# Kernel optimization log

Measured on AMD Instinct MI355X. Metric: run time of the kernel, lower is better.

Reference implementation:

```python
import jax, jax.numpy as jnp
import numpy as np

# Static tree structure: B jets, each a perfect binary tree of depth DEPTH.
B = 64
DEPTH = 12                       # levels 0..DEPTH; level j has B*2**j nodes
N_FEAT = 7
N_HID = 128
LEVEL_SIZES = [B * (1 << j) for j in range(DEPTH + 1)]
OFFSETS = np.concatenate([[0], np.cumsum(LEVEL_SIZES)]).astype(np.int64).tolist()
TOTAL = OFFSETS[-1]              # 524224 nodes
INNER_SIZES = LEVEL_SIZES[:-1]   # all nodes inner except leaf level
INNER_OFF = np.concatenate([[0], np.cumsum(INNER_SIZES)]).astype(np.int64).tolist()


def setup_inputs() -> dict:
    key = jax.random.key(0)
    k_c, k_wu, k_wh = jax.random.split(key, 3)
    contents = jax.random.normal(k_c, (TOTAL, N_FEAT), dtype=jnp.float32)
    # children: per level j < DEPTH, a random pairing (permutation) of level j+1 nodes
    rng = np.random.default_rng(0)
    ch = []
    for j in range(DEPTH):
        perm = rng.permutation(LEVEL_SIZES[j + 1]).astype(np.int32)
        ch.append(perm.reshape(LEVEL_SIZES[j], 2))
    children = jnp.asarray(np.concatenate(ch, axis=0))  # [262080, 2]
    # Learned params (torch nn.Linear: y = x @ W.T + b)
    w_u = jax.random.normal(k_wu, (N_HID, N_FEAT), dtype=jnp.float32) / np.float32(np.sqrt(N_FEAT))
    b_u = jnp.zeros((N_HID,), jnp.float32)
    w_h = jax.random.normal(k_wh, (N_HID, 3 * N_HID), dtype=jnp.float32) / np.float32(np.sqrt(3 * N_HID))
    b_h = jnp.zeros((N_HID,), jnp.float32)
    return {"contents": contents, "children": children,
            "w_u": w_u, "b_u": b_u, "w_h": w_h, "b_h": b_h}


def reference(contents, children, w_u, b_u, w_h, b_h):
    # Bottom-up pass over tree levels (leaves -> root), mirroring the torch loop
    # over levels[::-1]. Perfect binary tree: every non-leaf node is inner.
    emb = None
    for j in range(DEPTH, -1, -1):
        c_j = contents[OFFSETS[j]:OFFSETS[j + 1]]              # [B*2^j, F]
        u = jnp.tanh(c_j @ w_u.T + b_u)                        # [B*2^j, H]
        if j < DEPTH:
            ch_j = children[INNER_OFF[j]:INNER_OFF[j + 1]]     # [B*2^j, 2]
            h_L = emb[ch_j[:, 0]]                              # gather from prev level
            h_R = emb[ch_j[:, 1]]
            emb = jnp.tanh(jnp.concatenate([h_L, h_R, u], axis=1) @ w_h.T + b_h)
        else:
            emb = u  # leaf level: no inner nodes
    return emb.reshape(B, -1)  # root embedding per jet: [B, N_HID]
```

## Files before the change

### kernel.cpp

```cpp
#include <hip/hip_runtime.h>
#include <hip/hip_bf16.h>


#define NF 7
#define NH 128
#define XSTR 136
#define XSTR3 392

typedef __bf16 bf16;
typedef __bf16 bf16x8 __attribute__((ext_vector_type(8)));
typedef float floatx16 __attribute__((ext_vector_type(16)));

__device__ __forceinline__ float ftanh(float x){
    float e = __expf(2.0f * x);
    return 1.0f - __fdividef(2.0f, e + 1.0f);
}

__global__ __launch_bounds__(256) void k_prep(
    const float* __restrict__ contents, const int2* __restrict__ children,
    const float* __restrict__ w_u, const float* __restrict__ b_u,
    const float* __restrict__ w_h,
    unsigned int* __restrict__ usm_u32, int* __restrict__ ids_A,
    int* __restrict__ ids_B, bf16* __restrict__ wb, bf16* __restrict__ w_ub)
{
    __shared__ float csL[128 * 8];
    const int t = threadIdx.x;
    const int b = blockIdx.x;

    if (b >= 512){
        if (b == 512){
            if (t < 64){
                int root = t;
                int* base = ids_B + root * 32;
                const int2* ch0 = children;
                const int2* ch1 = children + 64;
                const int2* ch2 = children + 192;
                const int2* ch3 = children + 448;
                int l1[2], l2[4], l3[8];
                { int2 c = ch0[root]; l1[0] = c.x; l1[1] = c.y; }
                #pragma unroll
                for (int k = 0; k < 2; ++k){ int2 c = ch1[l1[k]]; l2[2*k] = c.x; l2[2*k+1] = c.y; }
                #pragma unroll
                for (int k = 0; k < 4; ++k){ int2 c = ch2[l2[k]]; l3[2*k] = c.x; l3[2*k+1] = c.y; }
                base[0] = root;
                base[1] = l1[0]; base[2] = l1[1];
                #pragma unroll
                for (int k = 0; k < 4; ++k) base[3 + k] = l2[k];
                #pragma unroll
                for (int k = 0; k < 8; ++k) base[7 + k] = l3[k];
                #pragma unroll
                for (int k = 0; k < 8; ++k){
                    int2 c = ch3[l3[k]];
                    base[15 + 2*k] = c.x; base[16 + 2*k] = c.y;
                }
            } else if (t < 192){
                int col = t - 64;
                union { uint4 u4[2]; bf16 h[16]; } row;
                #pragma unroll
                for (int f = 0; f < NF; ++f) row.h[f] = (bf16)w_u[col * NF + f];
                row.h[7] = (bf16)b_u[col];
                #pragma unroll
                for (int k = 8; k < 16; ++k) row.h[k] = (bf16)0.0f;
                *(uint4*)&w_ub[col * 16]     = row.u4[0];
                *(uint4*)&w_ub[col * 16 + 8] = row.u4[1];
            }
        } else if (b < 517){
            int root = (b - 513) * 256 + t;
            int* base = ids_A + root * 128;
            const int2* ch4 = children + 960;
            const int2* ch5 = children + 1984;
            const int2* ch6 = children + 4032;
            const int2* ch7 = children + 8128;
            const int2* ch8 = children + 16320;
            const int2* ch9 = children + 32704;
            int l5[2], l6[4], l7[8], l8[16], l9[32];
            { int2 c = ch4[root]; l5[0] = c.x; l5[1] = c.y; }
            #pragma unroll
            for (int k = 0; k < 2; ++k){ int2 c = ch5[l5[k]]; l6[2*k] = c.x; l6[2*k+1] = c.y; }
            #pragma unroll
            for (int k = 0; k < 4; ++k){ int2 c = ch6[l6[k]]; l7[2*k] = c.x; l7[2*k+1] = c.y; }
            #pragma unroll
            for (int k = 0; k < 8; ++k){ int2 c = ch7[l7[k]]; l8[2*k] = c.x; l8[2*k+1] = c.y; }
            #pragma unroll
            for (int k = 0; k < 16; ++k){ int2 c = ch8[l8[k]]; l9[2*k] = c.x; l9[2*k+1] = c.y; }
            base[0] = root;
            base[1] = l5[0]; base[2] = l5[1];
            #pragma unroll
            for (int k = 0; k < 4; ++k)  base[3 + k]  = l6[k];
            #pragma unroll
            for (int k = 0; k < 8; ++k)  base[7 + k]  = l7[k];
            #pragma unroll
            for (int k = 0; k < 16; ++k) base[15 + k] = l8[k];
            #pragma unroll
            for (int k = 0; k < 32; ++k) base[31 + k] = l9[k];
            #pragma unroll
            for (int k = 0; k < 32; ++k){
                int2 c = ch9[l9[k]];
                base[63 + 2*k] = c.x; base[64 + 2*k] = c.y;
            }
        } else {
            int idx = (b - 517) * 256 + t;
            wb[idx] = (bf16)w_h[idx];
        }
        return;
    }

    const size_t srow = (size_t)b * 128;
    if (t < 224){
        float4 v = ((const float4*)(contents + srow * NF))[t];
        int e = t * 4;
        float vv[4] = {v.x, v.y, v.z, v.w};
        #pragma unroll
        for (int r = 0; r < 4; ++r){ int ee = e + r; csL[(ee/7)*8 + (ee%7)] = vv[r]; }
    }
    const int cp = t & 63;
    const int quarter = t >> 6;
    float wu0[NF], wu1[NF];
    const float* w0 = w_u + (size_t)(2 * cp) * NF;
    #pragma unroll
    for (int f = 0; f < NF; ++f){ wu0[f] = w0[f]; wu1[f] = w0[NF + f]; }
    const float bu0 = b_u[2 * cp], bu1 = b_u[2 * cp + 1];
    __syncthreads();
    #pragma unroll 4
    for (int i = 0; i < 32; ++i){
        int node = quarter * 32 + i;
        float4 c0 = *(const float4*)&csL[node * 8];
        float4 c1 = *(const float4*)&csL[node * 8 + 4];
        float a0 = bu0, a1 = bu1;
        a0 = fmaf(c0.x, wu0[0], a0); a1 = fmaf(c0.x, wu1[0], a1);
        a0 = fmaf(c0.y, wu0[1], a0); a1 = fmaf(c0.y, wu1[1], a1);
        a0 = fmaf(c0.z, wu0[2], a0); a1 = fmaf(c0.z, wu1[2], a1);
        a0 = fmaf(c0.w, wu0[3], a0); a1 = fmaf(c0.w, wu1[3], a1);
        a0 = fmaf(c1.x, wu0[4], a0); a1 = fmaf(c1.x, wu1[4], a1);
        a0 = fmaf(c1.y, wu0[5], a0); a1 = fmaf(c1.y, wu1[5], a1);
        a0 = fmaf(c1.z, wu0[6], a0); a1 = fmaf(c1.z, wu1[6], a1);
        union { unsigned int u; bf16 h[2]; } pk;
        pk.h[0] = (bf16)ftanh(a0);
        pk.h[1] = (bf16)ftanh(a1);
        usm_u32[(srow + node) * 64 + cp] = pk.u;
    }
}

__global__ __launch_bounds__(256, 2) void k_lvl11(
    const float* __restrict__ contents, const int2* __restrict__ children,
    const bf16* __restrict__ w_ub, const bf16* __restrict__ wb,
    const float* __restrict__ b_h, bf16* __restrict__ emb11)
{
    __shared__ bf16 xs[64 * XSTR3];
    __shared__ bf16 ca[192 * 16];
    __shared__ int chS[128];
    const int t = threadIdx.x;
    const int node0 = blockIdx.x * 64;
    const int2* ch11 = children + 131008;
    const float* cont11 = contents + (size_t)131008 * NF;
    const float* contL  = contents + (size_t)262080 * NF;

    if (t < 64){ int2 c = ch11[node0 + t]; chS[2*t] = c.x; chS[2*t + 1] = c.y; }
    __syncthreads();

    if (t < 192){
        const float* src = (t < 128) ? (contL + (size_t)chS[t] * NF)
                                     : (cont11 + (size_t)(node0 + t - 128) * NF);
        union { uint4 u4[2]; bf16 h[16]; } row;
        #pragma unroll
        for (int f = 0; f < NF; ++f) row.h[f] = (bf16)src[f];
        row.h[7] = (bf16)1.0f;
        #pragma unroll
        for (int k = 8; k < 16; ++k) row.h[k] = (bf16)0.0f;
        *(uint4*)&ca[t * 16]     = row.u4[0];
        *(uint4*)&ca[t * 16 + 8] = row.u4[1];
    }

    const int lane = t & 63;
    const int ct = t >> 6;
    const int m = lane & 31;
    const int q = lane >> 5;
    const int colg = ct * 32 + m;
    const bf16x8 bu = *(const bf16x8*)(w_ub + (size_t)colg * 16 + q * 8);
    __syncthreads();

    #pragma unroll
    for (int tile = 0; tile < 6; ++tile){
        bf16x8 a = *(const bf16x8*)&ca[(tile * 32 + m) * 16 + q * 8];
        floatx16 acc = {0,0,0,0,0,0,0,0,0,0,0,0,0,0,0,0};
        acc = __builtin_amdgcn_mfma_f32_32x32x16_bf16(a, bu, acc, 0, 0, 0);
        #pragma unroll
        for (int r = 0; r < 16; ++r){
            int row = (r & 3) + 8 * (r >> 2) + 4 * q;
            bf16 hv = (bf16)ftanh(acc[r]);
            if (tile < 4){
                int c = tile * 32 + row;
                xs[(c >> 1) * XSTR3 + (c & 1) * 128 + colg] = hv;
            } else {
                int i = (tile - 4) * 32 + row;
                xs[i * XSTR3 + 256 + colg] = hv;
            }
        }
    }
    __syncthreads();

    floatx16 acc0 = {0,0,0,0,0,0,0,0,0,0,0,0,0,0,0,0};
    floatx16 acc1 = {0,0,0,0,0,0,0,0,0,0,0,0,0,0,0,0};
    const bf16* bq = wb + (size_t)colg * 384 + q * 8;
    const bf16* xa = &xs[m * XSTR3 + q * 8];
    #pragma unroll
    for (int grp = 0; grp < 3; ++grp){
        bf16x8 bfr[8];
        #pragma unroll
        for (int kk = 0; kk < 8; ++kk)
            bfr[kk] = *(const bf16x8*)(bq + grp * 128 + kk * 16);
        #pragma unroll
        for (int kk = 0; kk < 8; ++kk){
            bf16x8 a0 = *(const bf16x8*)(xa + grp * 128 + kk * 16);
            bf16x8 a1 = *(const bf16x8*)(xa + grp * 128 + kk * 16 + 32 * XSTR3);
            acc0 = __builtin_amdgcn_mfma_f32_32x32x16_bf16(a0, bfr[kk], acc0, 0, 0, 0);
            acc1 = __builtin_amdgcn_mfma_f32_32x32x16_bf16(a1, bfr[kk], acc1, 0, 0, 0);
        }
    }

    const float bv = b_h[colg];
    #pragma unroll
    for (int nt = 0; nt < 2; ++nt){
        const floatx16* accp = nt ? &acc1 : &acc0;
        #pragma unroll
        for (int r = 0; r < 16; ++r){
            int row  = (r & 3) + 8 * (r >> 2) + 4 * q;
            int node = node0 + nt * 32 + row;
            emb11[(size_t)node * NH + colg] = (bf16)ftanh((*accp)[r] + bv);
        }
    }
}

__global__ __launch_bounds__(256, 4) void k_inner(
    const int2* __restrict__ children, const float* __restrict__ contents,
    const float* __restrict__ w_u, const float* __restrict__ b_u,
    const bf16* __restrict__ wb, const float* __restrict__ b_h,
    const bf16* __restrict__ emb_next, bf16* __restrict__ out_b)
{
    __shared__ bf16 xs[64 * XSTR];
    __shared__ int2 ch_s[64];
    __shared__ float cs[64 * 8];
    const int t = threadIdx.x;
    const int block0 = blockIdx.x * 64;
    if (t < 64) ch_s[t] = children[block0 + t];
    if (t < 112){
        float4 v = ((const float4*)(contents + (size_t)block0 * NF))[t];
        int e = t * 4;
        float vv[4] = {v.x, v.y, v.z, v.w};
        #pragma unroll
        for (int r = 0; r < 4; ++r){ int ee = e + r; cs[(ee/7)*8 + (ee%7)] = vv[r]; }
    }
    const int cp = t & 63;
    const int quarter = t >> 6;
    float wu0[NF], wu1[NF];
    {
        const float* w0 = w_u + (size_t)(2 * cp) * NF;
        #pragma unroll
        for (int f = 0; f < NF; ++f){ wu0[f] = w0[f]; wu1[f] = w0[NF + f]; }
    }
    const float bu0 = b_u[2 * cp], bu1 = b_u[2 * cp + 1];
    const int lane = t & 63;
    const int ct = t >> 6;
    const int m = lane & 31;
    const int q = lane >> 5;
    floatx16 acc0 = {0,0,0,0,0,0,0,0,0,0,0,0,0,0,0,0};
    floatx16 acc1 = {0,0,0,0,0,0,0,0,0,0,0,0,0,0,0,0};
    const bf16* bq = wb + ((size_t)(ct * 32 + m) * 384 + q * 8);
    #pragma unroll 1
    for (int p = 0; p < 3; ++p){
        __syncthreads();
        if (p < 2){
            #pragma unroll
            for (int r = 0; r < 4; ++r){
                int task = r * 256 + t;
                int i = task >> 4, part = task & 15;
                int row = (p == 0) ? ch_s[i].x : ch_s[i].y;
                uint4 v = *(const uint4*)(emb_next + (size_t)row * NH + part * 8);
                *(uint4*)&xs[i * XSTR + part * 8] = v;
            }
        } else {
            #pragma unroll 4
            for (int i = 0; i < 16; ++i){
                int node = quarter * 16 + i;
                float4 c0 = *(const float4*)&cs[node * 8];
                float4 c1 = *(const float4*)&cs[node * 8 + 4];
                float a0 = bu0, a1 = bu1;
                a0 = fmaf(c0.x, wu0[0], a0); a1 = fmaf(c0.x, wu1[0], a1);
                a0 = fmaf(c0.y, wu0[1], a0); a1 = fmaf(c0.y, wu1[1], a1);
                a0 = fmaf(c0.z, wu0[2], a0); a1 = fmaf(c0.z, wu1[2], a1);
                a0 = fmaf(c0.w, wu0[3], a0); a1 = fmaf(c0.w, wu1[3], a1);
                a0 = fmaf(c1.x, wu0[4], a0); a1 = fmaf(c1.x, wu1[4], a1);
                a0 = fmaf(c1.y, wu0[5], a0); a1 = fmaf(c1.y, wu1[5], a1);
                a0 = fmaf(c1.z, wu0[6], a0); a1 = fmaf(c1.z, wu1[6], a1);
                union { unsigned int u; bf16 h[2]; } pk;
                pk.h[0] = (bf16)ftanh(a0);
                pk.h[1] = (bf16)ftanh(a1);
                ((unsigned int*)xs)[node * (XSTR / 2) + cp] = pk.u;
            }
        }
        bf16x8 bfr[8];
        #pragma unroll
        for (int kk = 0; kk < 8; ++kk)
            bfr[kk] = *(const bf16x8*)(bq + p * 128 + kk * 16);
        __syncthreads();
        const bf16* xa = &xs[m * XSTR + q * 8];
        #pragma unroll
        for (int kk = 0; kk < 8; ++kk){
            bf16x8 a0 = *(const bf16x8*)(xa + kk * 16);
            bf16x8 a1 = *(const bf16x8*)(xa + kk * 16 + 32 * XSTR);
            acc0 = __builtin_amdgcn_mfma_f32_32x32x16_bf16(a0, bfr[kk], acc0, 0, 0, 0);
            acc1 = __builtin_amdgcn_mfma_f32_32x32x16_bf16(a1, bfr[kk], acc1, 0, 0, 0);
        }
    }
    const int colg = ct * 32 + m;
    const float bv = b_h[colg];
    #pragma unroll
    for (int nt = 0; nt < 2; ++nt){
        const floatx16* accp = nt ? &acc1 : &acc0;
        #pragma unroll
        for (int r = 0; r < 16; ++r){
            int row  = (r & 3) + 8 * (r >> 2) + 4 * q;
            int node = block0 + nt * 32 + row;
            out_b[(size_t)node * NH + colg] = (bf16)ftanh((*accp)[r] + bv);
        }
    }
}

__global__ __launch_bounds__(256, 2) void k_tailA(
    const int* __restrict__ ids_A, const bf16* __restrict__ u_small,
    const bf16* __restrict__ wb, const float* __restrict__ b_h,
    const bf16* __restrict__ emb10, bf16* __restrict__ emb4)
{
    __shared__ bf16 xs[32 * XSTR3];
    __shared__ bf16 embL[32 * 136];
    __shared__ int ids[128];
    const int t = threadIdx.x, root = blockIdx.x;
    const int ct = t >> 6, lane = t & 63, m = lane & 31, q = lane >> 5;
    const float bv = b_h[ct * 32 + m];
    if (t < 32) ((uint4*)ids)[t] = ((const uint4*)(ids_A + root * 128))[t];
    __syncthreads();
    const bf16* bq = wb + ((size_t)(ct * 32 + m) * 384 + q * 8);

    #pragma unroll 1
    for (int l = 9; l >= 4; --l){
        const int n = 1 << (l - 4);
        #pragma unroll 1
        for (int r = 0; r < 4; ++r){
            int task = r * 256 + t;
            if (task < n * 32){
                int i = task >> 5, half = (task >> 4) & 1, part = task & 15;
                uint4 v;
                if (l == 9) v = *(const uint4*)(emb10 + (size_t)ids[63 + 2*i + half] * NH + part * 8);
                else        v = *(uint4*)&embL[(2*i + half) * 136 + part * 8];
                *(uint4*)&xs[i * XSTR3 + half * 128 + part * 8] = v;
            }
        }
        #pragma unroll 1
        for (int r = 0; r < 2; ++r){
            int task = r * 256 + t;
            if (task < n * 16){
                int i = task >> 4, part = task & 15;
                size_t row = (size_t)64 * ((1u << l) - 1) + ids[(n - 1) + i];
                *(uint4*)&xs[i * XSTR3 + 256 + part * 8] =
                    *(const uint4*)(u_small + row * NH + part * 8);
            }
        }
        __syncthreads();
        floatx16 accs[3];
        #pragma unroll
        for (int g = 0; g < 3; ++g) accs[g] = (floatx16){0,0,0,0,0,0,0,0,0,0,0,0,0,0,0,0};
        const bf16* xa = &xs[m * XSTR3 + q * 8];
        #pragma unroll
        for (int grp = 0; grp < 3; ++grp){
            bf16x8 bfr[8];
            #pragma unroll
            for (int kk = 0; kk < 8; ++kk)
                bfr[kk] = *(const bf16x8*)(bq + grp * 128 + kk * 16);
            #pragma unroll
            for (int kk = 0; kk < 8; ++kk){
                bf16x8 a0 = *(const bf16x8*)(xa + grp * 128 + kk * 16);
                accs[grp] = __builtin_amdgcn_mfma_f32_32x32x16_bf16(a0, bfr[kk], accs[grp], 0, 0, 0);
            }
        }
        floatx16 acc = accs[0] + accs[1] + accs[2];
        __syncthreads();
        #pragma unroll
        for (int r = 0; r < 16; ++r){
            int row = (r & 3) + 8 * (r >> 2) + 4 * q;
            if (row < n){
                float v = ftanh(acc[r] + bv);
                if (l > 4) embL[row * 136 + ct * 32 + m] = (bf16)v;
                else       emb4[(size_t)root * NH + ct * 32 + m] = (bf16)v;
            }
        }
        __syncthreads();
    }
}

__global__ __launch_bounds__(256, 2) void k_tailB(
    const int* __restrict__ ids_B, const bf16* __restrict__ u_small,
    const bf16* __restrict__ wb, const float* __restrict__ b_h,
    const bf16* __restrict__ emb4, float* __restrict__ out_f)
{
    __shared__ bf16 xs[8 * XSTR3];
    __shared__ bf16 embL[8 * 136];
    __shared__ int ids[32];
    const int t = threadIdx.x, root = blockIdx.x;
    const int ct = t >> 6, lane = t & 63, m = lane & 31, q = lane >> 5;
    const float bv = b_h[ct * 32 + m];
    if (t < 8) ((uint4*)ids)[t] = ((const uint4*)(ids_B + root * 32))[t];
    __syncthreads();
    const bf16* bq = wb + ((size_t)(ct * 32 + m) * 384 + q * 8);

    #pragma unroll 1
    for (int l = 3; l >= 0; --l){
        const int n = 1 << l;
        {
            int task = t;
            if (task < n * 32){
                int i = task >> 5, half = (task >> 4) & 1, part = task & 15;
                uint4 v;
                if (l == 3) v = *(const uint4*)(emb4 + (size_t)ids[15 + 2*i + half] * NH + part * 8);
                else        v = *(uint4*)&embL[(2*i + half) * 136 + part * 8];
                *(uint4*)&xs[i * XSTR3 + half * 128 + part * 8] = v;
            }
            if (task < n * 16){
                int i = task >> 4, part = task & 15;
                size_t row = (size_t)64 * ((1u << l) - 1) + ids[(n - 1) + i];
                *(uint4*)&xs[i * XSTR3 + 256 + part * 8] =
                    *(const uint4*)(u_small + row * NH + part * 8);
            }
        }
        __syncthreads();
        floatx16 accs[3];
        #pragma unroll
        for (int g = 0; g < 3; ++g) accs[g] = (floatx16){0,0,0,0,0,0,0,0,0,0,0,0,0,0,0,0};
        const bf16* xa = &xs[m * XSTR3 + q * 8];
        #pragma unroll
        for (int grp = 0; grp < 3; ++grp){
            bf16x8 bfr[8];
            #pragma unroll
            for (int kk = 0; kk < 8; ++kk)
                bfr[kk] = *(const bf16x8*)(bq + grp * 128 + kk * 16);
            #pragma unroll
            for (int kk = 0; kk < 8; ++kk){
                bf16x8 a0 = *(const bf16x8*)(xa + grp * 128 + kk * 16);
                accs[grp] = __builtin_amdgcn_mfma_f32_32x32x16_bf16(a0, bfr[kk], accs[grp], 0, 0, 0);
            }
        }
        floatx16 acc = accs[0] + accs[1] + accs[2];
        __syncthreads();
        #pragma unroll
        for (int r = 0; r < 16; ++r){
            int row = (r & 3) + 8 * (r >> 2) + 4 * q;
            if (row < n){
                float v = ftanh(acc[r] + bv);
                if (l > 0) embL[row * 136 + ct * 32 + m] = (bf16)v;
                else       out_f[(size_t)root * NH + ct * 32 + m] = v;
            }
        }
        __syncthreads();
    }
}

extern "C" void kernel_launch(void* const* d_in, const int* in_sizes, int n_in,
                              void* d_out, int out_size, void* d_ws, size_t ws_size,
                              hipStream_t stream){
    const float* contents = (const float*)d_in[0];
    const int2*  children = (const int2*)d_in[1];
    const float* w_u      = (const float*)d_in[2];
    const float* b_u      = (const float*)d_in[3];
    const float* w_h      = (const float*)d_in[4];
    const float* b_h      = (const float*)d_in[5];
    float* outf = (float*)d_out;

    bf16* embA    = (bf16*)d_ws;
    bf16* embB    = embA + (size_t)65536 * NH;
    bf16* wb      = embB + (size_t)131072 * NH;
    bf16* u_small = wb + (size_t)NH * 384;
    int*  ids_A   = (int*)(u_small + (size_t)65536 * NH);
    int*  ids_B   = ids_A + 1024 * 128;
    bf16* w_ub    = (bf16*)(ids_B + 64 * 32);

    hipLaunchKernelGGL(k_prep, dim3(709), dim3(256), 0, stream,
                       contents, children, w_u, b_u, w_h,
                       (unsigned int*)u_small, ids_A, ids_B, wb, w_ub);
    hipLaunchKernelGGL(k_lvl11, dim3(2048), dim3(256), 0, stream,
                       contents, children, w_ub, wb, b_h, embB);
    hipLaunchKernelGGL(k_inner, dim3(1024), dim3(256), 0, stream,
                       children + 65472, contents + (size_t)65472 * NF,
                       w_u, b_u, wb, b_h, embB, embA);
    hipLaunchKernelGGL(k_tailA, dim3(1024), dim3(256), 0, stream,
                       ids_A, u_small, wb, b_h, embA, embB);
    hipLaunchKernelGGL(k_tailB, dim3(64), dim3(256), 0, stream,
                       ids_B, u_small, wb, b_h, embB, outf);
}
```

Measured before the change: 223.0 us.

## Fuse prep kernel into level-11 kernel and halve its node tile

Folds the separate preparation kernel (leaf u precompute, index tables, weight bf16 conversion) into the level-11 kernel as extra blocks, removing one launch and its dependency barrier. The level-11 blocks now convert w_u/b_u and w_h to bf16 on the fly from fp32 instead of reading prepared copies. Each block handles 32 nodes instead of 64, doubling the block count, so every block reloads and converts the full W_h slice and per-block weight reuse halves. Extra global traffic and conversion work per block are traded for fewer launches and more parallelism.

```diff
diff --git a/kernel.cpp b/kernel.cpp
--- a/kernel.cpp
+++ b/kernel.cpp
@@ -16,19 +16,92 @@
     return 1.0f - __fdividef(2.0f, e + 1.0f);
 }
 
-__global__ __launch_bounds__(256) void k_prep(
+__global__ __launch_bounds__(256, 2) void k_lvl11(
     const float* __restrict__ contents, const int2* __restrict__ children,
     const float* __restrict__ w_u, const float* __restrict__ b_u,
-    const float* __restrict__ w_h,
+    const float* __restrict__ w_h, const float* __restrict__ b_h,
+    bf16* __restrict__ emb11,
     unsigned int* __restrict__ usm_u32, int* __restrict__ ids_A,
-    int* __restrict__ ids_B, bf16* __restrict__ wb, bf16* __restrict__ w_ub)
+    int* __restrict__ ids_B, bf16* __restrict__ wb)
 {
-    __shared__ float csL[128 * 8];
+    __shared__ bf16 xs[32 * XSTR3];
+    __shared__ bf16 ca[96 * 16];
+    __shared__ int chS[64];
     const int t = threadIdx.x;
     const int b = blockIdx.x;
 
-    if (b >= 512){
-        if (b == 512){
+    if (b >= 4096){
+        if (b < 4608){
+            float* csL = (float*)xs;
+            const size_t srow = (size_t)(b - 4096) * 128;
+            if (t < 224){
+                float4 v = ((const float4*)(contents + srow * NF))[t];
+                int e = t * 4;
+                float vv[4] = {v.x, v.y, v.z, v.w};
+                #pragma unroll
+                for (int r = 0; r < 4; ++r){ int ee = e + r; csL[(ee/7)*8 + (ee%7)] = vv[r]; }
+            }
+            const int cp = t & 63;
+            const int quarter = t >> 6;
+            float wu0[NF], wu1[NF];
+            const float* w0 = w_u + (size_t)(2 * cp) * NF;
+            #pragma unroll
+            for (int f = 0; f < NF; ++f){ wu0[f] = w0[f]; wu1[f] = w0[NF + f]; }
+            const float bu0 = b_u[2 * cp], bu1 = b_u[2 * cp + 1];
+            __syncthreads();
+            #pragma unroll 4
+            for (int i = 0; i < 32; ++i){
+                int node = quarter * 32 + i;
+                float4 c0 = *(const float4*)&csL[node * 8];
+                float4 c1 = *(const float4*)&csL[node * 8 + 4];
+                float a0 = bu0, a1 = bu1;
+                a0 = fmaf(c0.x, wu0[0], a0); a1 = fmaf(c0.x, wu1[0], a1);
+                a0 = fmaf(c0.y, wu0[1], a0); a1 = fmaf(c0.y, wu1[1], a1);
+                a0 = fmaf(c0.z, wu0[2], a0); a1 = fmaf(c0.z, wu1[2], a1);
+                a0 = fmaf(c0.w, wu0[3], a0); a1 = fmaf(c0.w, wu1[3], a1);
+                a0 = fmaf(c1.x, wu0[4], a0); a1 = fmaf(c1.x, wu1[4], a1);
+                a0 = fmaf(c1.y, wu0[5], a0); a1 = fmaf(c1.y, wu1[5], a1);
+                a0 = fmaf(c1.z, wu0[6], a0); a1 = fmaf(c1.z, wu1[6], a1);
+                union { unsigned int u; bf16 h[2]; } pk;
+                pk.h[0] = (bf16)ftanh(a0);
+                pk.h[1] = (bf16)ftanh(a1);
+                usm_u32[(srow + node) * 64 + cp] = pk.u;
+            }
+        } else if (b < 4612){
+            int root = (b - 4608) * 256 + t;
+            int* base = ids_A + root * 128;
+            const int2* ch4 = children + 960;
+            const int2* ch5 = children + 1984;
+            const int2* ch6 = children + 4032;
+            const int2* ch7 = children + 8128;
+            const int2* ch8 = children + 16320;
+            const int2* ch9 = children + 32704;
+            int l5[2], l6[4], l7[8], l8[16], l9[32];
+            { int2 c = ch4[root]; l5[0] = c.x; l5[1] = c.y; }
+            #pragma unroll
+            for (int k = 0; k < 2; ++k){ int2 c = ch5[l5[k]]; l6[2*k] = c.x; l6[2*k+1] = c.y; }
+            #pragma unroll
+            for (int k = 0; k < 4; ++k){ int2 c = ch6[l6[k]]; l7[2*k] = c.x; l7[2*k+1] = c.y; }
+            #pragma unroll
+            for (int k = 0; k < 8; ++k){ int2 c = ch7[l7[k]]; l8[2*k] = c.x; l8[2*k+1] = c.y; }
+            #pragma unroll
+            for (int k = 0; k < 16; ++k){ int2 c = ch8[l8[k]]; l9[2*k] = c.x; l9[2*k+1] = c.y; }
+            base[0] = root;
+            base[1] = l5[0]; base[2] = l5[1];
+            #pragma unroll
+            for (int k = 0; k < 4; ++k)  base[3 + k]  = l6[k];
+            #pragma unroll
+            for (int k = 0; k < 8; ++k)  base[7 + k]  = l7[k];
+            #pragma unroll
+            for (int k = 0; k < 16; ++k) base[15 + k] = l8[k];
+            #pragma unroll
+            for (int k = 0; k < 32; ++k) base[31 + k] = l9[k];
+            #pragma unroll
+            for (int k = 0; k < 32; ++k){
+                int2 c = ch9[l9[k]];
+                base[63 + 2*k] = c.x; base[64 + 2*k] = c.y;
+            }
+        } else if (b == 4612){
             if (t < 64){
                 int root = t;
                 int* base = ids_B + root * 32;
@@ -53,114 +126,25 @@
                     int2 c = ch3[l3[k]];
                     base[15 + 2*k] = c.x; base[16 + 2*k] = c.y;
                 }
-            } else if (t < 192){
-                int col = t - 64;
-                union { uint4 u4[2]; bf16 h[16]; } row;
-                #pragma unroll
-                for (int f = 0; f < NF; ++f) row.h[f] = (bf16)w_u[col * NF + f];
-                row.h[7] = (bf16)b_u[col];
-                #pragma unroll
-                for (int k = 8; k < 16; ++k) row.h[k] = (bf16)0.0f;
-                *(uint4*)&w_ub[col * 16]     = row.u4[0];
-                *(uint4*)&w_ub[col * 16 + 8] = row.u4[1];
-            }
-        } else if (b < 517){
-            int root = (b - 513) * 256 + t;
-            int* base = ids_A + root * 128;
-            const int2* ch4 = children + 960;
-            const int2* ch5 = children + 1984;
-            const int2* ch6 = children + 4032;
-            const int2* ch7 = children + 8128;
-            const int2* ch8 = children + 16320;
-            const int2* ch9 = children + 32704;
-            int l5[2], l6[4], l7[8], l8[16], l9[32];
-            { int2 c = ch4[root]; l5[0] = c.x; l5[1] = c.y; }
-            #pragma unroll
-            for (int k = 0; k < 2; ++k){ int2 c = ch5[l5[k]]; l6[2*k] = c.x; l6[2*k+1] = c.y; }
-            #pragma unroll
-            for (int k = 0; k < 4; ++k){ int2 c = ch6[l6[k]]; l7[2*k] = c.x; l7[2*k+1] = c.y; }
-            #pragma unroll
-            for (int k = 0; k < 8; ++k){ int2 c = ch7[l7[k]]; l8[2*k] = c.x; l8[2*k+1] = c.y; }
-            #pragma unroll
-            for (int k = 0; k < 16; ++k){ int2 c = ch8[l8[k]]; l9[2*k] = c.x; l9[2*k+1] = c.y; }
-            base[0] = root;
-            base[1] = l5[0]; base[2] = l5[1];
-            #pragma unroll
-            for (int k = 0; k < 4; ++k)  base[3 + k]  = l6[k];
-            #pragma unroll
-            for (int k = 0; k < 8; ++k)  base[7 + k]  = l7[k];
-            #pragma unroll
-            for (int k = 0; k < 16; ++k) base[15 + k] = l8[k];
-            #pragma unroll
-            for (int k = 0; k < 32; ++k) base[31 + k] = l9[k];
-            #pragma unroll
-            for (int k = 0; k < 32; ++k){
-                int2 c = ch9[l9[k]];
-                base[63 + 2*k] = c.x; base[64 + 2*k] = c.y;
             }
         } else {
-            int idx = (b - 517) * 256 + t;
+            int idx = (b - 4613) * 256 + t;
             wb[idx] = (bf16)w_h[idx];
         }
         return;
     }
 
-    const size_t srow = (size_t)b * 128;
-    if (t < 224){
-        float4 v = ((const float4*)(contents + srow * NF))[t];
-        int e = t * 4;
-        float vv[4] = {v.x, v.y, v.z, v.w};
-        #pragma unroll
-        for (int r = 0; r < 4; ++r){ int ee = e + r; csL[(ee/7)*8 + (ee%7)] = vv[r]; }
-    }
-    const int cp = t & 63;
-    const int quarter = t >> 6;
-    float wu0[NF], wu1[NF];
-    const float* w0 = w_u + (size_t)(2 * cp) * NF;
-    #pragma unroll
-    for (int f = 0; f < NF; ++f){ wu0[f] = w0[f]; wu1[f] = w0[NF + f]; }
-    const float bu0 = b_u[2 * cp], bu1 = b_u[2 * cp + 1];
-    __syncthreads();
-    #pragma unroll 4
-    for (int i = 0; i < 32; ++i){
-        int node = quarter * 32 + i;
-        float4 c0 = *(const float4*)&csL[node * 8];
-        float4 c1 = *(const float4*)&csL[node * 8 + 4];
-        float a0 = bu0, a1 = bu1;
-        a0 = fmaf(c0.x, wu0[0], a0); a1 = fmaf(c0.x, wu1[0], a1);
-        a0 = fmaf(c0.y, wu0[1], a0); a1 = fmaf(c0.y, wu1[1], a1);
-        a0 = fmaf(c0.z, wu0[2], a0); a1 = fmaf(c0.z, wu1[2], a1);
-        a0 = fmaf(c0.w, wu0[3], a0); a1 = fmaf(c0.w, wu1[3], a1);
-        a0 = fmaf(c1.x, wu0[4], a0); a1 = fmaf(c1.x, wu1[4], a1);
-        a0 = fmaf(c1.y, wu0[5], a0); a1 = fmaf(c1.y, wu1[5], a1);
-        a0 = fmaf(c1.z, wu0[6], a0); a1 = fmaf(c1.z, wu1[6], a1);
-        union { unsigned int u; bf16 h[2]; } pk;
-        pk.h[0] = (bf16)ftanh(a0);
-        pk.h[1] = (bf16)ftanh(a1);
-        usm_u32[(srow + node) * 64 + cp] = pk.u;
-    }
-}
-
-__global__ __launch_bounds__(256, 2) void k_lvl11(
-    const float* __restrict__ contents, const int2* __restrict__ children,
-    const bf16* __restrict__ w_ub, const bf16* __restrict__ wb,
-    const float* __restrict__ b_h, bf16* __restrict__ emb11)
-{
-    __shared__ bf16 xs[64 * XSTR3];
-    __shared__ bf16 ca[192 * 16];
-    __shared__ int chS[128];
-    const int t = threadIdx.x;
-    const int node0 = blockIdx.x * 64;
+    const int node0 = b * 32;
     const int2* ch11 = children + 131008;
     const float* cont11 = contents + (size_t)131008 * NF;
     const float* contL  = contents + (size_t)262080 * NF;
 
-    if (t < 64){ int2 c = ch11[node0 + t]; chS[2*t] = c.x; chS[2*t + 1] = c.y; }
+    if (t < 32){ int2 c = ch11[node0 + t]; chS[2*t] = c.x; chS[2*t + 1] = c.y; }
     __syncthreads();
 
-    if (t < 192){
-        const float* src = (t < 128) ? (contL + (size_t)chS[t] * NF)
-                                     : (cont11 + (size_t)(node0 + t - 128) * NF);
+    if (t < 96){
+        const float* src = (t < 64) ? (contL + (size_t)chS[t] * NF)
+                                    : (cont11 + (size_t)(node0 + t - 64) * NF);
         union { uint4 u4[2]; bf16 h[16]; } row;
         #pragma unroll
         for (int f = 0; f < NF; ++f) row.h[f] = (bf16)src[f];
@@ -176,11 +160,21 @@
     const int m = lane & 31;
     const int q = lane >> 5;
     const int colg = ct * 32 + m;
-    const bf16x8 bu = *(const bf16x8*)(w_ub + (size_t)colg * 16 + q * 8);
+    const float bv = b_h[colg];
+
+    bf16x8 bu = {bf16(0.f),bf16(0.f),bf16(0.f),bf16(0.f),
+                 bf16(0.f),bf16(0.f),bf16(0.f),bf16(0.f)};
+    if (q == 0){
+        union { bf16x8 v; bf16 h[8]; } u8;
+        #pragma unroll
+        for (int f = 0; f < NF; ++f) u8.h[f] = (bf16)w_u[colg * NF + f];
+        u8.h[7] = (bf16)b_u[colg];
+        bu = u8.v;
+    }
     __syncthreads();
 
     #pragma unroll
-    for (int tile = 0; tile < 6; ++tile){
+    for (int tile = 0; tile < 3; ++tile){
         bf16x8 a = *(const bf16x8*)&ca[(tile * 32 + m) * 16 + q * 8];
         floatx16 acc = {0,0,0,0,0,0,0,0,0,0,0,0,0,0,0,0};
         acc = __builtin_amdgcn_mfma_f32_32x32x16_bf16(a, bu, acc, 0, 0, 0);
@@ -188,46 +182,45 @@
         for (int r = 0; r < 16; ++r){
             int row = (r & 3) + 8 * (r >> 2) + 4 * q;
             bf16 hv = (bf16)ftanh(acc[r]);
-            if (tile < 4){
+            if (tile < 2){
                 int c = tile * 32 + row;
                 xs[(c >> 1) * XSTR3 + (c & 1) * 128 + colg] = hv;
             } else {
-                int i = (tile - 4) * 32 + row;
-                xs[i * XSTR3 + 256 + colg] = hv;
+                xs[row * XSTR3 + 256 + colg] = hv;
             }
         }
     }
     __syncthreads();
 
     floatx16 acc0 = {0,0,0,0,0,0,0,0,0,0,0,0,0,0,0,0};
-    floatx16 acc1 = {0,0,0,0,0,0,0,0,0,0,0,0,0,0,0,0};
-    const bf16* bq = wb + (size_t)colg * 384 + q * 8;
+    const float* bqf = w_h + (size_t)colg * 384 + q * 8;
     const bf16* xa = &xs[m * XSTR3 + q * 8];
     #pragma unroll
     for (int grp = 0; grp < 3; ++grp){
         bf16x8 bfr[8];
         #pragma unroll
-        for (int kk = 0; kk < 8; ++kk)
-            bfr[kk] = *(const bf16x8*)(bq + grp * 128 + kk * 16);
+        for (int kk = 0; kk < 8; ++kk){
+            float4 f0 = *(const float4*)(bqf + grp * 128 + kk * 16);
+            float4 f1 = *(const float4*)(bqf + grp * 128 + kk * 16 + 4);
+            union { bf16x8 v; bf16 h[8]; } u8;
+            u8.h[0] = (bf16)f0.x; u8.h[1] = (bf16)f0.y;
+            u8.h[2] = (bf16)f0.z; u8.h[3] = (bf16)f0.w;
+            u8.h[4] = (bf16)f1.x; u8.h[5] = (bf16)f1.y;
+            u8.h[6] = (bf16)f1.z; u8.h[7] = (bf16)f1.w;
+            bfr[kk] = u8.v;
+        }
         #pragma unroll
         for (int kk = 0; kk < 8; ++kk){
             bf16x8 a0 = *(const bf16x8*)(xa + grp * 128 + kk * 16);
-            bf16x8 a1 = *(const bf16x8*)(xa + grp * 128 + kk * 16 + 32 * XSTR3);
             acc0 = __builtin_amdgcn_mfma_f32_32x32x16_bf16(a0, bfr[kk], acc0, 0, 0, 0);
-            acc1 = __builtin_amdgcn_mfma_f32_32x32x16_bf16(a1, bfr[kk], acc1, 0, 0, 0);
-        }
-    }
-
-    const float bv = b_h[colg];
+        }
+    }
+
     #pragma unroll
-    for (int nt = 0; nt < 2; ++nt){
-        const floatx16* accp = nt ? &acc1 : &acc0;
-        #pragma unroll
-        for (int r = 0; r < 16; ++r){
-            int row  = (r & 3) + 8 * (r >> 2) + 4 * q;
-            int node = node0 + nt * 32 + row;
-            emb11[(size_t)node * NH + colg] = (bf16)ftanh((*accp)[r] + bv);
-        }
+    for (int r = 0; r < 16; ++r){
+        int row  = (r & 3) + 8 * (r >> 2) + 4 * q;
+        int node = node0 + row;
+        emb11[(size_t)node * NH + colg] = (bf16)ftanh(acc0[r] + bv);
     }
 }
 
@@ -480,13 +473,10 @@
     bf16* u_small = wb + (size_t)NH * 384;
     int*  ids_A   = (int*)(u_small + (size_t)65536 * NH);
     int*  ids_B   = ids_A + 1024 * 128;
-    bf16* w_ub    = (bf16*)(ids_B + 64 * 32);
-
-    hipLaunchKernelGGL(k_prep, dim3(709), dim3(256), 0, stream,
-                       contents, children, w_u, b_u, w_h,
-                       (unsigned int*)u_small, ids_A, ids_B, wb, w_ub);
-    hipLaunchKernelGGL(k_lvl11, dim3(2048), dim3(256), 0, stream,
-                       contents, children, w_ub, wb, b_h, embB);
+
+    hipLaunchKernelGGL(k_lvl11, dim3(4805), dim3(256), 0, stream,
+                       contents, children, w_u, b_u, w_h, b_h,
+                       embB, (unsigned int*)u_small, ids_A, ids_B, wb);
     hipLaunchKernelGGL(k_inner, dim3(1024), dim3(256), 0, stream,
                        children + 65472, contents + (size_t)65472 * NF,
                        w_u, b_u, wb, b_h, embB, embA);
```

New measurement: 269.4 us. 20.8% more time.

## Fuse level-10 inner pass and both tail kernels into one persistent kernel

Applied to the files above, without the earlier changes.

Removes the separate level-10 inner kernel and merges the two tail kernels into a single persistent kernel of 256 blocks. Each block processes whole subtrees from level 10 down to level 4 in shared memory, then a global atomic barrier hands off to the top-level pass. The prep kernel is widened to precompute 256-entry subtree index lists and extra u rows for level 10. This removes two kernel launches and the global round trip of level-10 embeddings. In exchange there is less parallelism for level 10 and a spin barrier whose reset logic depends on a sentinel value in the workspace.

```diff
diff --git a/kernel.cpp b/kernel.cpp
--- a/kernel.cpp
+++ b/kernel.cpp
@@ -4,7 +4,6 @@
 
 #define NF 7
 #define NH 128
-#define XSTR 136
 #define XSTR3 392
 
 typedef __bf16 bf16;
@@ -27,8 +26,47 @@
     const int t = threadIdx.x;
     const int b = blockIdx.x;
 
-    if (b >= 512){
-        if (b == 512){
+    if (b >= 1024){
+        if (b < 1028){
+            int root = (b - 1024) * 256 + t;
+            int* base = ids_A + root * 256;
+            const int2* ch4  = children + 960;
+            const int2* ch5  = children + 1984;
+            const int2* ch6  = children + 4032;
+            const int2* ch7  = children + 8128;
+            const int2* ch8  = children + 16320;
+            const int2* ch9  = children + 32704;
+            const int2* ch10 = children + 65472;
+            int l5[2], l6[4], l7[8], l8[16], l9[32], l10[64];
+            { int2 c = ch4[root]; l5[0] = c.x; l5[1] = c.y; }
+            #pragma unroll
+            for (int k = 0; k < 2; ++k){ int2 c = ch5[l5[k]]; l6[2*k] = c.x; l6[2*k+1] = c.y; }
+            #pragma unroll
+            for (int k = 0; k < 4; ++k){ int2 c = ch6[l6[k]]; l7[2*k] = c.x; l7[2*k+1] = c.y; }
+            #pragma unroll
+            for (int k = 0; k < 8; ++k){ int2 c = ch7[l7[k]]; l8[2*k] = c.x; l8[2*k+1] = c.y; }
+            #pragma unroll
+            for (int k = 0; k < 16; ++k){ int2 c = ch8[l8[k]]; l9[2*k] = c.x; l9[2*k+1] = c.y; }
+            #pragma unroll
+            for (int k = 0; k < 32; ++k){ int2 c = ch9[l9[k]]; l10[2*k] = c.x; l10[2*k+1] = c.y; }
+            base[0] = root;
+            base[1] = l5[0]; base[2] = l5[1];
+            #pragma unroll
+            for (int k = 0; k < 4; ++k)  base[3 + k]  = l6[k];
+            #pragma unroll
+            for (int k = 0; k < 8; ++k)  base[7 + k]  = l7[k];
+            #pragma unroll
+            for (int k = 0; k < 16; ++k) base[15 + k] = l8[k];
+            #pragma unroll
+            for (int k = 0; k < 32; ++k) base[31 + k] = l9[k];
+            #pragma unroll
+            for (int k = 0; k < 64; ++k) base[63 + k] = l10[k];
+            #pragma unroll
+            for (int k = 0; k < 64; ++k){
+                int2 c = ch10[l10[k]];
+                base[127 + 2*k] = c.x; base[128 + 2*k] = c.y;
+            }
+        } else if (b == 1028){
             if (t < 64){
                 int root = t;
                 int* base = ids_B + root * 32;
@@ -64,42 +102,8 @@
                 *(uint4*)&w_ub[col * 16]     = row.u4[0];
                 *(uint4*)&w_ub[col * 16 + 8] = row.u4[1];
             }
-        } else if (b < 517){
-            int root = (b - 513) * 256 + t;
-            int* base = ids_A + root * 128;
-            const int2* ch4 = children + 960;
-            const int2* ch5 = children + 1984;
-            const int2* ch6 = children + 4032;
-            const int2* ch7 = children + 8128;
-            const int2* ch8 = children + 16320;
-            const int2* ch9 = children + 32704;
-            int l5[2], l6[4], l7[8], l8[16], l9[32];
-            { int2 c = ch4[root]; l5[0] = c.x; l5[1] = c.y; }
-            #pragma unroll
-            for (int k = 0; k < 2; ++k){ int2 c = ch5[l5[k]]; l6[2*k] = c.x; l6[2*k+1] = c.y; }
-            #pragma unroll
-            for (int k = 0; k < 4; ++k){ int2 c = ch6[l6[k]]; l7[2*k] = c.x; l7[2*k+1] = c.y; }
-            #pragma unroll
-            for (int k = 0; k < 8; ++k){ int2 c = ch7[l7[k]]; l8[2*k] = c.x; l8[2*k+1] = c.y; }
-            #pragma unroll
-            for (int k = 0; k < 16; ++k){ int2 c = ch8[l8[k]]; l9[2*k] = c.x; l9[2*k+1] = c.y; }
-            base[0] = root;
-            base[1] = l5[0]; base[2] = l5[1];
-            #pragma unroll
-            for (int k = 0; k < 4; ++k)  base[3 + k]  = l6[k];
-            #pragma unroll
-            for (int k = 0; k < 8; ++k)  base[7 + k]  = l7[k];
-            #pragma unroll
-            for (int k = 0; k < 16; ++k) base[15 + k] = l8[k];
-            #pragma unroll
-            for (int k = 0; k < 32; ++k) base[31 + k] = l9[k];
-            #pragma unroll
-            for (int k = 0; k < 32; ++k){
-                int2 c = ch9[l9[k]];
-                base[63 + 2*k] = c.x; base[64 + 2*k] = c.y;
-            }
         } else {
-            int idx = (b - 517) * 256 + t;
+            int idx = (b - 1029) * 256 + t;
             wb[idx] = (bf16)w_h[idx];
         }
         return;
@@ -231,235 +235,151 @@
     }
 }
 
-__global__ __launch_bounds__(256, 4) void k_inner(
-    const int2* __restrict__ children, const float* __restrict__ contents,
-    const float* __restrict__ w_u, const float* __restrict__ b_u,
-    const bf16* __restrict__ wb, const float* __restrict__ b_h,
-    const bf16* __restrict__ emb_next, bf16* __restrict__ out_b)
+__global__ __launch_bounds__(256, 2) void k_tail(
+    const int* __restrict__ ids_A, const int* __restrict__ ids_B,
+    const bf16* __restrict__ u_small, const bf16* __restrict__ wb,
+    const float* __restrict__ b_h, const bf16* __restrict__ emb11,
+    bf16* __restrict__ emb4, float* __restrict__ out_f,
+    unsigned int* __restrict__ bar)
 {
-    __shared__ bf16 xs[64 * XSTR];
-    __shared__ int2 ch_s[64];
-    __shared__ float cs[64 * 8];
+    __shared__ bf16 xs[64 * XSTR3];
+    __shared__ bf16 embL[64 * 136];
+    __shared__ int ids[256];
     const int t = threadIdx.x;
-    const int block0 = blockIdx.x * 64;
-    if (t < 64) ch_s[t] = children[block0 + t];
-    if (t < 112){
-        float4 v = ((const float4*)(contents + (size_t)block0 * NF))[t];
-        int e = t * 4;
-        float vv[4] = {v.x, v.y, v.z, v.w};
-        #pragma unroll
-        for (int r = 0; r < 4; ++r){ int ee = e + r; cs[(ee/7)*8 + (ee%7)] = vv[r]; }
-    }
-    const int cp = t & 63;
-    const int quarter = t >> 6;
-    float wu0[NF], wu1[NF];
-    {
-        const float* w0 = w_u + (size_t)(2 * cp) * NF;
-        #pragma unroll
-        for (int f = 0; f < NF; ++f){ wu0[f] = w0[f]; wu1[f] = w0[NF + f]; }
-    }
-    const float bu0 = b_u[2 * cp], bu1 = b_u[2 * cp + 1];
-    const int lane = t & 63;
-    const int ct = t >> 6;
-    const int m = lane & 31;
-    const int q = lane >> 5;
-    floatx16 acc0 = {0,0,0,0,0,0,0,0,0,0,0,0,0,0,0,0};
-    floatx16 acc1 = {0,0,0,0,0,0,0,0,0,0,0,0,0,0,0,0};
-    const bf16* bq = wb + ((size_t)(ct * 32 + m) * 384 + q * 8);
+    const int ct = t >> 6, lane = t & 63, m = lane & 31, q = lane >> 5;
+    const int colg = ct * 32 + m;
+    const float bv = b_h[colg];
+    const bf16* bq = wb + (size_t)colg * 384 + q * 8;
+
     #pragma unroll 1
-    for (int p = 0; p < 3; ++p){
+    for (int root = blockIdx.x; root < 1024; root += 256){
         __syncthreads();
-        if (p < 2){
-            #pragma unroll
+        if (t < 64) ((uint4*)ids)[t] = ((const uint4*)(ids_A + root * 256))[t];
+        __syncthreads();
+        #pragma unroll 1
+        for (int l = 10; l >= 4; --l){
+            const int n = 1 << (l - 4);
+            #pragma unroll 1
+            for (int r = 0; r < 8; ++r){
+                int task = r * 256 + t;
+                if (task < n * 32){
+                    int i = task >> 5, half = (task >> 4) & 1, part = task & 15;
+                    uint4 v;
+                    if (l == 10) v = *(const uint4*)(emb11 + (size_t)ids[127 + 2*i + half] * NH + part * 8);
+                    else         v = *(uint4*)&embL[(2*i + half) * 136 + part * 8];
+                    *(uint4*)&xs[i * XSTR3 + half * 128 + part * 8] = v;
+                }
+            }
+            #pragma unroll 1
             for (int r = 0; r < 4; ++r){
                 int task = r * 256 + t;
-                int i = task >> 4, part = task & 15;
-                int row = (p == 0) ? ch_s[i].x : ch_s[i].y;
-                uint4 v = *(const uint4*)(emb_next + (size_t)row * NH + part * 8);
-                *(uint4*)&xs[i * XSTR + part * 8] = v;
-            }
-        } else {
-            #pragma unroll 4
-            for (int i = 0; i < 16; ++i){
-                int node = quarter * 16 + i;
-                float4 c0 = *(const float4*)&cs[node * 8];
-                float4 c1 = *(const float4*)&cs[node * 8 + 4];
-                float a0 = bu0, a1 = bu1;
-                a0 = fmaf(c0.x, wu0[0], a0); a1 = fmaf(c0.x, wu1[0], a1);
-                a0 = fmaf(c0.y, wu0[1], a0); a1 = fmaf(c0.y, wu1[1], a1);
-                a0 = fmaf(c0.z, wu0[2], a0); a1 = fmaf(c0.z, wu1[2], a1);
-                a0 = fmaf(c0.w, wu0[3], a0); a1 = fmaf(c0.w, wu1[3], a1);
-                a0 = fmaf(c1.x, wu0[4], a0); a1 = fmaf(c1.x, wu1[4], a1);
-                a0 = fmaf(c1.y, wu0[5], a0); a1 = fmaf(c1.y, wu1[5], a1);
-                a0 = fmaf(c1.z, wu0[6], a0); a1 = fmaf(c1.z, wu1[6], a1);
-                union { unsigned int u; bf16 h[2]; } pk;
-                pk.h[0] = (bf16)ftanh(a0);
-                pk.h[1] = (bf16)ftanh(a1);
-                ((unsigned int*)xs)[node * (XSTR / 2) + cp] = pk.u;
-            }
-        }
-        bf16x8 bfr[8];
-        #pragma unroll
-        for (int kk = 0; kk < 8; ++kk)
-            bfr[kk] = *(const bf16x8*)(bq + p * 128 + kk * 16);
+                if (task < n * 16){
+                    int i = task >> 4, part = task & 15;
+                    size_t row = (size_t)64 * ((1u << l) - 1) + ids[(n - 1) + i];
+                    *(uint4*)&xs[i * XSTR3 + 256 + part * 8] =
+                        *(const uint4*)(u_small + row * NH + part * 8);
+                }
+            }
+            __syncthreads();
+            const int ntc = (n + 31) >> 5;
+            #pragma unroll 1
+            for (int nt = 0; nt < ntc; ++nt){
+                floatx16 accs[3];
+                #pragma unroll
+                for (int g = 0; g < 3; ++g) accs[g] = (floatx16){0,0,0,0,0,0,0,0,0,0,0,0,0,0,0,0};
+                const bf16* xa = &xs[(nt * 32 + m) * XSTR3 + q * 8];
+                #pragma unroll
+                for (int grp = 0; grp < 3; ++grp){
+                    bf16x8 bfr[8];
+                    #pragma unroll
+                    for (int kk = 0; kk < 8; ++kk)
+                        bfr[kk] = *(const bf16x8*)(bq + grp * 128 + kk * 16);
+                    #pragma unroll
+                    for (int kk = 0; kk < 8; ++kk){
+                        bf16x8 a0 = *(const bf16x8*)(xa + grp * 128 + kk * 16);
+                        accs[grp] = __builtin_amdgcn_mfma_f32_32x32x16_bf16(a0, bfr[kk], accs[grp], 0, 0, 0);
+                    }
+                }
+                floatx16 acc = accs[0] + accs[1] + accs[2];
+                #pragma unroll
+                for (int r = 0; r < 16; ++r){
+                    int row = nt * 32 + (r & 3) + 8 * (r >> 2) + 4 * q;
+                    if (row < n){
+                        float v = ftanh(acc[r] + bv);
+                        if (l > 4) embL[row * 136 + colg] = (bf16)v;
+                        else       emb4[(size_t)root * NH + colg] = (bf16)v;
+                    }
+                }
+            }
+            __syncthreads();
+        }
+    }
+
+    __threadfence();
+    __syncthreads();
+    if (t == 0){
+        unsigned int expected = 0xAAAAAAAAu;
+        __hip_atomic_compare_exchange_strong(bar, &expected, 0u,
+            __ATOMIC_ACQ_REL, __ATOMIC_RELAXED, __HIP_MEMORY_SCOPE_AGENT);
+        __hip_atomic_fetch_add(bar, 1u, __ATOMIC_ACQ_REL, __HIP_MEMORY_SCOPE_AGENT);
+        while (__hip_atomic_load(bar, __ATOMIC_ACQUIRE, __HIP_MEMORY_SCOPE_AGENT) < 256u)
+            __builtin_amdgcn_s_sleep(8);
+    }
+    __syncthreads();
+
+    if (blockIdx.x < 64){
+        const int root = blockIdx.x;
+        if (t < 8) ((uint4*)ids)[t] = ((const uint4*)(ids_B + root * 32))[t];
         __syncthreads();
-        const bf16* xa = &xs[m * XSTR + q * 8];
-        #pragma unroll
-        for (int kk = 0; kk < 8; ++kk){
-            bf16x8 a0 = *(const bf16x8*)(xa + kk * 16);
-            bf16x8 a1 = *(const bf16x8*)(xa + kk * 16 + 32 * XSTR);
-            acc0 = __builtin_amdgcn_mfma_f32_32x32x16_bf16(a0, bfr[kk], acc0, 0, 0, 0);
-            acc1 = __builtin_amdgcn_mfma_f32_32x32x16_bf16(a1, bfr[kk], acc1, 0, 0, 0);
-        }
-    }
-    const int colg = ct * 32 + m;
-    const float bv = b_h[colg];
-    #pragma unroll
-    for (int nt = 0; nt < 2; ++nt){
-        const floatx16* accp = nt ? &acc1 : &acc0;
-        #pragma unroll
-        for (int r = 0; r < 16; ++r){
-            int row  = (r & 3) + 8 * (r >> 2) + 4 * q;
-            int node = block0 + nt * 32 + row;
-            out_b[(size_t)node * NH + colg] = (bf16)ftanh((*accp)[r] + bv);
-        }
-    }
-}
-
-__global__ __launch_bounds__(256, 2) void k_tailA(
-    const int* __restrict__ ids_A, const bf16* __restrict__ u_small,
-    const bf16* __restrict__ wb, const float* __restrict__ b_h,
-    const bf16* __restrict__ emb10, bf16* __restrict__ emb4)
-{
-    __shared__ bf16 xs[32 * XSTR3];
-    __shared__ bf16 embL[32 * 136];
-    __shared__ int ids[128];
-    const int t = threadIdx.x, root = blockIdx.x;
-    const int ct = t >> 6, lane = t & 63, m = lane & 31, q = lane >> 5;
-    const float bv = b_h[ct * 32 + m];
-    if (t < 32) ((uint4*)ids)[t] = ((const uint4*)(ids_A + root * 128))[t];
-    __syncthreads();
-    const bf16* bq = wb + ((size_t)(ct * 32 + m) * 384 + q * 8);
-
-    #pragma unroll 1
-    for (int l = 9; l >= 4; --l){
-        const int n = 1 << (l - 4);
         #pragma unroll 1
-        for (int r = 0; r < 4; ++r){
-            int task = r * 256 + t;
-            if (task < n * 32){
-                int i = task >> 5, half = (task >> 4) & 1, part = task & 15;
-                uint4 v;
-                if (l == 9) v = *(const uint4*)(emb10 + (size_t)ids[63 + 2*i + half] * NH + part * 8);
-                else        v = *(uint4*)&embL[(2*i + half) * 136 + part * 8];
-                *(uint4*)&xs[i * XSTR3 + half * 128 + part * 8] = v;
-            }
-        }
-        #pragma unroll 1
-        for (int r = 0; r < 2; ++r){
-            int task = r * 256 + t;
-            if (task < n * 16){
-                int i = task >> 4, part = task & 15;
-                size_t row = (size_t)64 * ((1u << l) - 1) + ids[(n - 1) + i];
-                *(uint4*)&xs[i * XSTR3 + 256 + part * 8] =
-                    *(const uint4*)(u_small + row * NH + part * 8);
-            }
-        }
-        __syncthreads();
-        floatx16 accs[3];
-        #pragma unroll
-        for (int g = 0; g < 3; ++g) accs[g] = (floatx16){0,0,0,0,0,0,0,0,0,0,0,0,0,0,0,0};
-        const bf16* xa = &xs[m * XSTR3 + q * 8];
-        #pragma unroll
-        for (int grp = 0; grp < 3; ++grp){
-            bf16x8 bfr[8];
-            #pragma unroll
-            for (int kk = 0; kk < 8; ++kk)
-                bfr[kk] = *(const bf16x8*)(bq + grp * 128 + kk * 16);
-            #pragma unroll
-            for (int kk = 0; kk < 8; ++kk){
-                bf16x8 a0 = *(const bf16x8*)(xa + grp * 128 + kk * 16);
-                accs[grp] = __builtin_amdgcn_mfma_f32_32x32x16_bf16(a0, bfr[kk], accs[grp], 0, 0, 0);
-            }
-        }
-        floatx16 acc = accs[0] + accs[1] + accs[2];
-        __syncthreads();
-        #pragma unroll
-        for (int r = 0; r < 16; ++r){
-            int row = (r & 3) + 8 * (r >> 2) + 4 * q;
-            if (row < n){
-                float v = ftanh(acc[r] + bv);
-                if (l > 4) embL[row * 136 + ct * 32 + m] = (bf16)v;
-                else       emb4[(size_t)root * NH + ct * 32 + m] = (bf16)v;
-            }
-        }
-        __syncthreads();
-    }
-}
-
-__global__ __launch_bounds__(256, 2) void k_tailB(
-    const int* __restrict__ ids_B, const bf16* __restrict__ u_small,
-    const bf16* __restrict__ wb, const float* __restrict__ b_h,
-    const bf16* __restrict__ emb4, float* __restrict__ out_f)
-{
-    __shared__ bf16 xs[8 * XSTR3];
-    __shared__ bf16 embL[8 * 136];
-    __shared__ int ids[32];
-    const int t = threadIdx.x, root = blockIdx.x;
-    const int ct = t >> 6, lane = t & 63, m = lane & 31, q = lane >> 5;
-    const float bv = b_h[ct * 32 + m];
-    if (t < 8) ((uint4*)ids)[t] = ((const uint4*)(ids_B + root * 32))[t];
-    __syncthreads();
-    const bf16* bq = wb + ((size_t)(ct * 32 + m) * 384 + q * 8);
-
-    #pragma unroll 1
-    for (int l = 3; l >= 0; --l){
-        const int n = 1 << l;
-        {
-            int task = t;
-            if (task < n * 32){
-                int i = task >> 5, half = (task >> 4) & 1, part = task & 15;
-                uint4 v;
-                if (l == 3) v = *(const uint4*)(emb4 + (size_t)ids[15 + 2*i + half] * NH + part * 8);
-                else        v = *(uint4*)&embL[(2*i + half) * 136 + part * 8];
-                *(uint4*)&xs[i * XSTR3 + half * 128 + part * 8] = v;
-            }
-            if (task < n * 16){
-                int i = task >> 4, part = task & 15;
-                size_t row = (size_t)64 * ((1u << l) - 1) + ids[(n - 1) + i];
-                *(uint4*)&xs[i * XSTR3 + 256 + part * 8] =
-                    *(const uint4*)(u_small + row * NH + part * 8);
-            }
-        }
-        __syncthreads();
-        floatx16 accs[3];
-        #pragma unroll
-        for (int g = 0; g < 3; ++g) accs[g] = (floatx16){0,0,0,0,0,0,0,0,0,0,0,0,0,0,0,0};
-        const bf16* xa = &xs[m * XSTR3 + q * 8];
-        #pragma unroll
-        for (int grp = 0; grp < 3; ++grp){
-            bf16x8 bfr[8];
-            #pragma unroll
-            for (int kk = 0; kk < 8; ++kk)
-                bfr[kk] = *(const bf16x8*)(bq + grp * 128 + kk * 16);
-            #pragma unroll
-            for (int kk = 0; kk < 8; ++kk){
-                bf16x8 a0 = *(const bf16x8*)(xa + grp * 128 + kk * 16);
-                accs[grp] = __builtin_amdgcn_mfma_f32_32x32x16_bf16(a0, bfr[kk], accs[grp], 0, 0, 0);
-            }
-        }
-        floatx16 acc = accs[0] + accs[1] + accs[2];
-        __syncthreads();
-        #pragma unroll
-        for (int r = 0; r < 16; ++r){
-            int row = (r & 3) + 8 * (r >> 2) + 4 * q;
-            if (row < n){
-                float v = ftanh(acc[r] + bv);
-                if (l > 0) embL[row * 136 + ct * 32 + m] = (bf16)v;
-                else       out_f[(size_t)root * NH + ct * 32 + m] = v;
-            }
-        }
-        __syncthreads();
+        for (int l = 3; l >= 0; --l){
+            const int n = 1 << l;
+            {
+                int task = t;
+                if (task < n * 32){
+                    int i = task >> 5, half = (task >> 4) & 1, part = task & 15;
+                    uint4 v;
+                    if (l == 3) v = *(const uint4*)(emb4 + (size_t)ids[15 + 2*i + half] * NH + part * 8);
+                    else        v = *(uint4*)&embL[(2*i + half) * 136 + part * 8];
+                    *(uint4*)&xs[i * XSTR3 + half * 128 + part * 8] = v;
+                }
+                if (task < n * 16){
+                    int i = task >> 4, part = task & 15;
+                    size_t row = (size_t)64 * ((1u << l) - 1) + ids[(n - 1) + i];
+                    *(uint4*)&xs[i * XSTR3 + 256 + part * 8] =
+                        *(const uint4*)(u_small + row * NH + part * 8);
+                }
+            }
+            __syncthreads();
+            floatx16 accs[3];
+            #pragma unroll
+            for (int g = 0; g < 3; ++g) accs[g] = (floatx16){0,0,0,0,0,0,0,0,0,0,0,0,0,0,0,0};
+            const bf16* xa = &xs[m * XSTR3 + q * 8];
+            #pragma unroll
+            for (int grp = 0; grp < 3; ++grp){
+                bf16x8 bfr[8];
+                #pragma unroll
+                for (int kk = 0; kk < 8; ++kk)
+                    bfr[kk] = *(const bf16x8*)(bq + grp * 128 + kk * 16);
+                #pragma unroll
+                for (int kk = 0; kk < 8; ++kk){
+                    bf16x8 a0 = *(const bf16x8*)(xa + grp * 128 + kk * 16);
+                    accs[grp] = __builtin_amdgcn_mfma_f32_32x32x16_bf16(a0, bfr[kk], accs[grp], 0, 0, 0);
+                }
+            }
+            floatx16 acc = accs[0] + accs[1] + accs[2];
+            __syncthreads();
+            #pragma unroll
+            for (int r = 0; r < 16; ++r){
+                int row = (r & 3) + 8 * (r >> 2) + 4 * q;
+                if (row < n){
+                    float v = ftanh(acc[r] + bv);
+                    if (l > 0) embL[row * 136 + colg] = (bf16)v;
+                    else       out_f[(size_t)root * NH + colg] = v;
+                }
+            }
+            __syncthreads();
+        }
     }
 }
 
@@ -474,24 +394,20 @@
     const float* b_h      = (const float*)d_in[5];
     float* outf = (float*)d_out;
 
-    bf16* embA    = (bf16*)d_ws;
-    bf16* embB    = embA + (size_t)65536 * NH;
-    bf16* wb      = embB + (size_t)131072 * NH;
+    bf16* emb11   = (bf16*)d_ws;
+    bf16* emb4    = emb11 + (size_t)131072 * NH;
+    bf16* wb      = emb4 + (size_t)1024 * NH;
     bf16* u_small = wb + (size_t)NH * 384;
-    int*  ids_A   = (int*)(u_small + (size_t)65536 * NH);
-    int*  ids_B   = ids_A + 1024 * 128;
+    int*  ids_A   = (int*)(u_small + (size_t)131072 * NH);
+    int*  ids_B   = ids_A + 1024 * 256;
     bf16* w_ub    = (bf16*)(ids_B + 64 * 32);
-
-    hipLaunchKernelGGL(k_prep, dim3(709), dim3(256), 0, stream,
+    unsigned int* bar = (unsigned int*)(w_ub + 128 * 16);
+
+    hipLaunchKernelGGL(k_prep, dim3(1221), dim3(256), 0, stream,
                        contents, children, w_u, b_u, w_h,
                        (unsigned int*)u_small, ids_A, ids_B, wb, w_ub);
     hipLaunchKernelGGL(k_lvl11, dim3(2048), dim3(256), 0, stream,
-                       contents, children, w_ub, wb, b_h, embB);
-    hipLaunchKernelGGL(k_inner, dim3(1024), dim3(256), 0, stream,
-                       children + 65472, contents + (size_t)65472 * NF,
-                       w_u, b_u, wb, b_h, embB, embA);
-    hipLaunchKernelGGL(k_tailA, dim3(1024), dim3(256), 0, stream,
-                       ids_A, u_small, wb, b_h, embA, embB);
-    hipLaunchKernelGGL(k_tailB, dim3(64), dim3(256), 0, stream,
-                       ids_B, u_small, wb, b_h, embB, outf);
+                       contents, children, w_ub, wb, b_h, emb11);
+    hipLaunchKernelGGL(k_tail, dim3(256), dim3(256), 0, stream,
+                       ids_A, ids_B, u_small, wb, b_h, emb11, emb4, outf, bar);
 }
```

New measurement: 386.5 us. 1.73x slower.
